# Kernel tuning notes

Hardware: AMD Instinct MI355X
Metric: run time of the kernel (lower is better)

The kernel has to match this reference:

```python
import jax, jax.numpy as jnp
import numpy as np

THRESH = 0.4


def setup_inputs() -> dict:
    key = jax.random.key(0)
    ks = jax.random.split(key, 8)
    B, N, C, H, O = 8, 16384, 640, 256, 128
    s = 0.02  # small init so sigmoid(logits) ~ 0.5 -> realistic mixed selection
    return {
        "point_features": jax.random.normal(ks[0], (B, N, C), jnp.float32),
        "point_coords": jax.random.normal(ks[1], (B, N, 3), jnp.float32) * 10.0,
        "w1": jax.random.normal(ks[2], (C, H), jnp.float32) * s,
        "b1": jnp.zeros((H,), jnp.float32),
        "w2": jax.random.normal(ks[3], (H, 1), jnp.float32) * s,
        "b2": jnp.zeros((1,), jnp.float32),
        "wo": jax.random.normal(ks[4], (C, O), jnp.float32) * s,
        "bo": jnp.zeros((O,), jnp.float32),
    }


def reference(point_features, point_coords, w1, b1, w2, b2, wo, bo):
    B, N, _ = point_features.shape
    # 2-layer MLP -> per-point logit -> sigmoid score
    h = jax.nn.relu(jnp.einsum('bnc,ch->bnh', point_features, w1) + b1)
    logits = jnp.einsum('bnh,ho->bno', h, w2) + b2          # [B, N, 1]
    scores = jax.nn.sigmoid(logits)                          # [B, N, 1]
    # score-scaled features through output projection
    feats = jnp.einsum('bnc,co->bno', point_features * scores, wo) + bo  # [B, N, O]
    # score-threshold selection + per-batch stream compaction into a
    # zero-padded tensor (padded to N, the jit-static worst case)
    sel = scores[..., 0] > THRESH                            # [B, N] bool
    pos = jnp.cumsum(sel.astype(jnp.int32), axis=1) - 1      # destination slot
    pos = jnp.where(sel, pos, N)                             # unselected -> OOB (dropped)
    bidx = jnp.arange(B)[:, None]
    selected_keypoints = jnp.zeros_like(feats).at[bidx, pos].set(feats, mode='drop')
    selected_coords = jnp.zeros_like(point_coords).at[bidx, pos].set(point_coords, mode='drop')
    # point_mask: True where the row is zero padding (matches (coords==0).sum(-1)!=0)
    point_mask = jnp.sum(selected_coords == 0, axis=-1) != 0
    return selected_keypoints, selected_coords, point_mask
```

## Files before the change

### kernel.cpp

```cpp
#include <hip/hip_runtime.h>
#include <hip/hip_bf16.h>


typedef __attribute__((ext_vector_type(8))) short short8v;
typedef __attribute__((ext_vector_type(4))) float f32x4;

#define M_TOTAL 131072
#define C_DIM 640
#define H_DIM 256
#define O_DIM 128
#define NCOMB 384
#define TM 64
#define KSTEPS 20
#define N_PTS 16384
#define TILES_PER_B 256
#define NTILES 2048
#define THRL -0.4054651081f
#define FIX_MARGIN 0.03f

#define OUT_COORD_OFF 16777216
#define OUT_MASK_OFF  17170432

#define WT_OFF     0u
#define TMASK_OFF  491520u
#define TAGG_OFF   507904u
#define TEXCL_OFF  516096u
#define COUNTS_OFF 524288u
#define G_OFF      1572864u

#define LGKMCNT0 asm volatile("s_waitcnt lgkmcnt(0)" ::: "memory")
#define SBAR __builtin_amdgcn_s_barrier()

__device__ __forceinline__ unsigned int f2bf_bits(float f) {
  unsigned int u = __builtin_bit_cast(unsigned int, f);
  return (u + 0x7fffu + ((u >> 16) & 1u)) >> 16;
}
__device__ __forceinline__ unsigned int pack_bf2(float lo, float hi) {
  return f2bf_bits(lo) | (f2bf_bits(hi) << 16);
}

__global__ __launch_bounds__(256) void convert_w(const float* __restrict__ w1,
                                                 const float* __restrict__ wo,
                                                 unsigned short* __restrict__ Wt2) {
  int o = blockIdx.x * 256 + threadIdx.x;
  if (o < NCOMB * C_DIM) {
    int e = o & 7;
    int g = o >> 3;
    int pp = g & 3;
    int qq = (g >> 2) & 15;
    int tc = g >> 6;
    int ct = tc % 24;
    int t = tc / 24;
    int k = t * 32 + pp * 8 + e;
    int n = ct * 16 + qq;
    float v = (n < H_DIM) ? w1[k * H_DIM + n] : wo[k * O_DIM + (n - H_DIM)];
    Wt2[o] = (unsigned short)f2bf_bits(v);
  }
}

__global__ __launch_bounds__(512, 4) void gemm_fused(
    const float* __restrict__ pf, const unsigned short* __restrict__ Wt2,
    const float* __restrict__ w1, const float* __restrict__ b1,
    const float* __restrict__ w2, const float* __restrict__ b2,
    const float* __restrict__ bo, unsigned long long* __restrict__ tmask,
    int* __restrict__ tagg, float* __restrict__ G) {
  __shared__ __align__(16) unsigned short As[3][2048];

  const int tid = threadIdx.x;
  const int lane = tid & 63;
  const int wv = tid >> 6;
  const int q = lane & 15;
  const int p = lane >> 4;
  const int tile = blockIdx.x;
  const int m0 = tile * TM;

  f32x4 acc[3][4];
#pragma unroll
  for (int i = 0; i < 3; ++i)
#pragma unroll
    for (int rt = 0; rt < 4; ++rt) acc[i][rt] = (f32x4){0.f, 0.f, 0.f, 0.f};

  const float* asrc = pf + (size_t)(m0 + (tid >> 3)) * C_DIM + (tid & 7) * 4;
  const int aphys = ((tid >> 1) ^ ((tid >> 4) & 3)) * 8 + (tid & 1) * 4;
  const int aswz = (q >> 1) & 3;

  const unsigned short* bbase = Wt2 + wv * 512 + q * 32 + p * 8;

  float4 Rcur;
  {
    float4 R0 = *(const float4*)(asrc);
    Rcur = *(const float4*)(asrc + 32);
    *(uint2*)&As[0][aphys] = make_uint2(pack_bf2(R0.x, R0.y), pack_bf2(R0.z, R0.w));
    LGKMCNT0;
    SBAR;
  }

  int scur = 0;
#pragma unroll 1
  for (int t = 0; t < KSTEPS; ++t) {
    const unsigned short* bp = bbase + (size_t)t * 12288;
    short8v bc0 = *(const short8v*)(bp);
    short8v bc1 = *(const short8v*)(bp + 4096);
    short8v bc2 = *(const short8v*)(bp + 8192);
    int snxt = scur + 1;
    if (snxt == 3) snxt = 0;
    if (t + 2 < KSTEPS) {
      float4 Rnext = *(const float4*)(asrc + (t + 2) * 32);
      *(uint2*)&As[snxt][aphys] =
          make_uint2(pack_bf2(Rcur.x, Rcur.y), pack_bf2(Rcur.z, Rcur.w));
      Rcur = Rnext;
    } else if (t + 1 < KSTEPS) {
      *(uint2*)&As[snxt][aphys] =
          make_uint2(pack_bf2(Rcur.x, Rcur.y), pack_bf2(Rcur.z, Rcur.w));
    }
    LGKMCNT0;
    SBAR;
    short8v af[4];
#pragma unroll
    for (int rt = 0; rt < 4; ++rt)
      af[rt] = *(const short8v*)&As[scur][((rt * 64 + q * 4 + p) ^ aswz) * 8];
    __builtin_amdgcn_s_setprio(1);
#pragma unroll
    for (int rt = 0; rt < 4; ++rt) {
      acc[0][rt] = __builtin_amdgcn_mfma_f32_16x16x32_bf16(af[rt], bc0, acc[0][rt], 0, 0, 0);
      acc[1][rt] = __builtin_amdgcn_mfma_f32_16x16x32_bf16(af[rt], bc1, acc[1][rt], 0, 0, 0);
      acc[2][rt] = __builtin_amdgcn_mfma_f32_16x16x32_bf16(af[rt], bc2, acc[2][rt], 0, 0, 0);
    }
    __builtin_amdgcn_s_setprio(0);
    scur = snxt;
  }
  __syncthreads();

  float* lpart = (float*)&As[0][0];
  float* llog = (float*)&As[1][0];
  float* srow = llog + 64;
  float* fsum = srow + 64;
  unsigned long long* s_fixmask = (unsigned long long*)(fsum + 4);

  float w2v[2], b1v[2];
#pragma unroll
  for (int i = 0; i < 2; ++i) {
    int col = (wv + 8 * i) * 16 + q;
    w2v[i] = w2[col];
    b1v[i] = b1[col];
  }
#pragma unroll
  for (int rt = 0; rt < 4; ++rt) {
    float pr[4] = {0.f, 0.f, 0.f, 0.f};
#pragma unroll
    for (int i = 0; i < 2; ++i)
#pragma unroll
      for (int r = 0; r < 4; ++r)
        pr[r] += fmaxf(acc[i][rt][r] + b1v[i], 0.f) * w2v[i];
#pragma unroll
    for (int mk = 1; mk < 16; mk <<= 1)
#pragma unroll
      for (int r = 0; r < 4; ++r) pr[r] += __shfl_xor(pr[r], mk);
    if (q == 0)
#pragma unroll
      for (int r = 0; r < 4; ++r) lpart[wv * 64 + rt * 16 + p * 4 + r] = pr[r];
  }
  __syncthreads();

  bool nf = false;
  if (wv == 0) {
    float lg = b2[0];
#pragma unroll
    for (int w = 0; w < 8; ++w) lg += lpart[w * 64 + tid];
    llog[tid] = lg;
    nf = fabsf(lg - THRL) < FIX_MARGIN;
  }
  unsigned long long fm = __ballot(nf);
  if (tid == 0) *s_fixmask = fm;
  __syncthreads();

  unsigned long long fixmask = *s_fixmask;
  while (fixmask) {
    int row = __ffsll(fixmask) - 1;
    fixmask &= fixmask - 1;
    if (tid < 256) {
      const float* prow = pf + (size_t)(m0 + row) * C_DIM;
      float a0 = 0.f, a1 = 0.f;
      for (int c = 0; c < C_DIM; c += 2) {
        a0 = fmaf(prow[c], w1[(size_t)c * H_DIM + tid], a0);
        a1 = fmaf(prow[c + 1], w1[(size_t)(c + 1) * H_DIM + tid], a1);
      }
      float v = fmaxf(a0 + a1 + b1[tid], 0.f) * w2[tid];
#pragma unroll
      for (int mk = 1; mk < 64; mk <<= 1) v += __shfl_xor(v, mk);
      if (lane == 0) fsum[wv] = v;
    }
    __syncthreads();
    if (tid == 0)
      llog[row] = fsum[0] + fsum[1] + fsum[2] + fsum[3] + b2[0];
    __syncthreads();
  }

  bool sel = false;
  float flog = 0.f;
  if (wv == 0) {
    flog = llog[tid];
    sel = flog > THRL;
  }
  unsigned long long selmask = __ballot(sel);
  if (wv == 0) {
    srow[tid] = 1.f / (1.f + expf(-flog));
    if (tid == 0) {
      tmask[tile] = selmask;
      tagg[tile] = __popcll(selmask);
    }
  }
  __syncthreads();

  {
    const int gcol = wv * 16 + q;
    const float bov = bo[gcol];
#pragma unroll
    for (int rt = 0; rt < 4; ++rt)
#pragma unroll
      for (int r = 0; r < 4; ++r) {
        int row = rt * 16 + p * 4 + r;
        G[(size_t)(m0 + row) * O_DIM + gcol] = fmaf(acc[2][rt][r], srow[row], bov);
      }
  }
}

__global__ __launch_bounds__(256) void scan_tiles(const int* __restrict__ tagg,
                                                  int* __restrict__ texcl,
                                                  int* __restrict__ counts) {
  __shared__ int wsum[4];
  const int c = blockIdx.x, t = threadIdx.x;
  const int lane = t & 63, w = t >> 6;
  int v = tagg[c * 256 + t];
  int inc = v;
#pragma unroll
  for (int d = 1; d < 64; d <<= 1) {
    int n = __shfl_up(inc, d);
    if (lane >= d) inc += n;
  }
  if (lane == 63) wsum[w] = inc;
  __syncthreads();
  int base = 0;
#pragma unroll
  for (int ww = 0; ww < 4; ++ww)
    if (ww < w) base += wsum[ww];
  texcl[c * 256 + t] = base + inc - v;
  if (t == 255) counts[c] = base + inc;
}

__global__ __launch_bounds__(512) void scatter(
    const float* __restrict__ G, const unsigned long long* __restrict__ tmask,
    const int* __restrict__ texcl, const float* __restrict__ pc,
    float* __restrict__ out) {
  const int tile = blockIdx.x;
  const int tid = threadIdx.x;
  const int lane = tid & 63;
  const int wv = tid >> 6;
  const unsigned long long mask = tmask[tile];
  const int base = (tile >> 8) * N_PTS + texcl[tile];
  const int m0 = tile * TM;
#pragma unroll
  for (int j = 0; j < 8; ++j) {
    const int row = wv * 8 + j;
    if (!((mask >> row) & 1ull)) continue;
    const int dst = base + __popcll(mask & ((1ull << row) - 1ull));
    const int m = m0 + row;
    float2 g = *(const float2*)(G + (size_t)m * O_DIM + lane * 2);
    *(float2*)(out + (size_t)dst * O_DIM + lane * 2) = g;
    if (lane == 0) {
      float c0 = pc[m * 3], c1 = pc[m * 3 + 1], c2 = pc[m * 3 + 2];
      float* oc = out + OUT_COORD_OFF;
      oc[dst * 3] = c0; oc[dst * 3 + 1] = c1; oc[dst * 3 + 2] = c2;
      out[OUT_MASK_OFF + dst] = (c0 == 0.f || c1 == 0.f || c2 == 0.f) ? 1.f : 0.f;
    }
  }
}

__global__ __launch_bounds__(256) void fill_tail(const int* __restrict__ counts,
                                                 float* __restrict__ out) {
  const int lane = threadIdx.x & 63;
  for (int m = blockIdx.x * 4 + (threadIdx.x >> 6); m < M_TOTAL; m += 8192) {
    int b = m >> 14, j = m & (N_PTS - 1);
    if (j < counts[b]) continue;
    *(float2*)(out + (size_t)m * O_DIM + lane * 2) = make_float2(0.f, 0.f);
    if (lane == 0) {
      float* oc = out + OUT_COORD_OFF;
      oc[m * 3] = 0.f; oc[m * 3 + 1] = 0.f; oc[m * 3 + 2] = 0.f;
      out[OUT_MASK_OFF + m] = 1.f;
    }
  }
}

extern "C" void kernel_launch(void* const* d_in, const int* in_sizes, int n_in,
                              void* d_out, int out_size, void* d_ws, size_t ws_size,
                              hipStream_t stream) {
  const float* pf = (const float*)d_in[0];
  const float* pc = (const float*)d_in[1];
  const float* w1 = (const float*)d_in[2];
  const float* b1 = (const float*)d_in[3];
  const float* w2 = (const float*)d_in[4];
  const float* b2 = (const float*)d_in[5];
  const float* wo = (const float*)d_in[6];
  const float* bo = (const float*)d_in[7];
  float* out = (float*)d_out;
  char* ws = (char*)d_ws;

  unsigned short* Wt2 = (unsigned short*)(ws + WT_OFF);
  unsigned long long* tmask = (unsigned long long*)(ws + TMASK_OFF);
  int* tagg = (int*)(ws + TAGG_OFF);
  int* texcl = (int*)(ws + TEXCL_OFF);
  int* counts = (int*)(ws + COUNTS_OFF);
  float* G = (float*)(ws + G_OFF);

  convert_w<<<960, 256, 0, stream>>>(w1, wo, Wt2);
  gemm_fused<<<NTILES, 512, 0, stream>>>(pf, Wt2, w1, b1, w2, b2, bo,
                                         tmask, tagg, G);
  scan_tiles<<<8, 256, 0, stream>>>(tagg, texcl, counts);
  scatter<<<NTILES, 512, 0, stream>>>(G, tmask, texcl, pc, out);
  fill_tail<<<2048, 256, 0, stream>>>(counts, out);
}
```

Baseline: 197.5 us.

## Switch fused GEMM to FP8 MFMA with register-resident weights and persistent blocks

Weights are quantized to FP8 (scaled by 64) and activations are converted to FP8 on the fly, so the GEMM uses 16x16x32 fp8 MFMA instead of bf16. Each of 256 persistent blocks of 768 threads keeps its full K slice of weights in registers and loops over eight 64-row tiles. The aim is to cut weight reloads and halve LDS and MFMA operand width. The cost is lower precision, which is offset by widening the exact-recompute margin near the threshold, plus much higher register pressure.

```diff
diff --git a/kernel.cpp b/kernel.cpp
--- a/kernel.cpp
+++ b/kernel.cpp
@@ -2,227 +2,230 @@
 #include <hip/hip_bf16.h>
 
 
-typedef __attribute__((ext_vector_type(8))) short short8v;
 typedef __attribute__((ext_vector_type(4))) float f32x4;
 
 #define M_TOTAL 131072
 #define C_DIM 640
 #define H_DIM 256
 #define O_DIM 128
-#define NCOMB 384
-#define TM 64
-#define KSTEPS 20
+#define KS 20
 #define N_PTS 16384
-#define TILES_PER_B 256
-#define NTILES 2048
+#define NBLOCKS 256
+#define NCHUNKS 2048
 #define THRL -0.4054651081f
-#define FIX_MARGIN 0.03f
+#define FIX_MARGIN 0.08f
+#define INV64 0.015625f
 
 #define OUT_COORD_OFF 16777216
 #define OUT_MASK_OFF  17170432
 
 #define WT_OFF     0u
-#define TMASK_OFF  491520u
-#define TAGG_OFF   507904u
-#define TEXCL_OFF  516096u
-#define COUNTS_OFF 524288u
+#define TMASK_OFF  262144u
+#define TAGG_OFF   278528u
+#define TEXCL_OFF  286720u
+#define COUNTS_OFF 294912u
 #define G_OFF      1572864u
 
 #define LGKMCNT0 asm volatile("s_waitcnt lgkmcnt(0)" ::: "memory")
 #define SBAR __builtin_amdgcn_s_barrier()
 
-__device__ __forceinline__ unsigned int f2bf_bits(float f) {
-  unsigned int u = __builtin_bit_cast(unsigned int, f);
-  return (u + 0x7fffu + ((u >> 16) & 1u)) >> 16;
-}
-__device__ __forceinline__ unsigned int pack_bf2(float lo, float hi) {
-  return f2bf_bits(lo) | (f2bf_bits(hi) << 16);
-}
-
 __global__ __launch_bounds__(256) void convert_w(const float* __restrict__ w1,
                                                  const float* __restrict__ wo,
-                                                 unsigned short* __restrict__ Wt2) {
-  int o = blockIdx.x * 256 + threadIdx.x;
-  if (o < NCOMB * C_DIM) {
-    int e = o & 7;
-    int g = o >> 3;
-    int pp = g & 3;
-    int qq = (g >> 2) & 15;
-    int tc = g >> 6;
-    int ct = tc % 24;
-    int t = tc / 24;
-    int k = t * 32 + pp * 8 + e;
-    int n = ct * 16 + qq;
-    float v = (n < H_DIM) ? w1[k * H_DIM + n] : wo[k * O_DIM + (n - H_DIM)];
-    Wt2[o] = (unsigned short)f2bf_bits(v);
-  }
-}
-
-__global__ __launch_bounds__(512, 4) void gemm_fused(
-    const float* __restrict__ pf, const unsigned short* __restrict__ Wt2,
+                                                 unsigned int* __restrict__ Wu) {
+  int i = blockIdx.x * 256 + threadIdx.x;
+  if (i >= 61440) return;
+  int g = i >> 1, h = i & 1;
+  int p = g & 3, q = (g >> 2) & 15, tc = g >> 6;
+  int ct = tc % 24, t = tc / 24;
+  int n = ct * 16 + q;
+  int kb = t * 32 + p * 8 + h * 4;
+  float v[4];
+#pragma unroll
+  for (int e = 0; e < 4; ++e) {
+    int k = kb + e;
+    v[e] = ((n < H_DIM) ? w1[k * H_DIM + n] : wo[k * O_DIM + (n - H_DIM)]) * 64.f;
+  }
+  unsigned int u = __builtin_amdgcn_cvt_pk_fp8_f32(v[0], v[1], 0, false);
+  u = __builtin_amdgcn_cvt_pk_fp8_f32(v[2], v[3], u, true);
+  Wu[i] = u;
+}
+
+__global__ __launch_bounds__(768, 3) void gemm_fused(
+    const float* __restrict__ pf, const unsigned char* __restrict__ Wf8,
     const float* __restrict__ w1, const float* __restrict__ b1,
     const float* __restrict__ w2, const float* __restrict__ b2,
     const float* __restrict__ bo, unsigned long long* __restrict__ tmask,
     int* __restrict__ tagg, float* __restrict__ G) {
-  __shared__ __align__(16) unsigned short As[3][2048];
+  __shared__ __align__(16) unsigned char As[3][2048];
+  __shared__ float lpart[8][64];
+  __shared__ float llog[64];
+  __shared__ float srow[64];
+  __shared__ float fsum[4];
+  __shared__ unsigned long long s_fm;
 
   const int tid = threadIdx.x;
   const int lane = tid & 63;
   const int wv = tid >> 6;
   const int q = lane & 15;
   const int p = lane >> 4;
-  const int tile = blockIdx.x;
-  const int m0 = tile * TM;
-
-  f32x4 acc[3][4];
-#pragma unroll
-  for (int i = 0; i < 3; ++i)
-#pragma unroll
-    for (int rt = 0; rt < 4; ++rt) acc[i][rt] = (f32x4){0.f, 0.f, 0.f, 0.f};
-
-  const float* asrc = pf + (size_t)(m0 + (tid >> 3)) * C_DIM + (tid & 7) * 4;
-  const int aphys = ((tid >> 1) ^ ((tid >> 4) & 3)) * 8 + (tid & 1) * 4;
-  const int aswz = (q >> 1) & 3;
-
-  const unsigned short* bbase = Wt2 + wv * 512 + q * 32 + p * 8;
-
-  float4 Rcur;
-  {
-    float4 R0 = *(const float4*)(asrc);
-    Rcur = *(const float4*)(asrc + 32);
-    *(uint2*)&As[0][aphys] = make_uint2(pack_bf2(R0.x, R0.y), pack_bf2(R0.z, R0.w));
+  const int blk = blockIdx.x;
+
+  const char* bb = (const char*)Wf8 + (size_t)(q * 4 + p) * 8 + (size_t)(2 * wv) * 512;
+  long B0[KS], B1[KS];
+#pragma unroll
+  for (int t = 0; t < KS; ++t) {
+    B0[t] = *(const long*)(bb + (size_t)t * 12288);
+    B1[t] = *(const long*)(bb + (size_t)t * 12288 + 512);
+  }
+
+  const int row_s = tid >> 3;
+  const int kh = tid & 7;
+  const int wboff = ((((kh >> 1) << 6) + row_s) ^ (kh >> 1)) * 8 + (kh & 1) * 4;
+
+#define STW(SLOT, F)                                                          \
+  {                                                                           \
+    unsigned int u_ = __builtin_amdgcn_cvt_pk_fp8_f32((F).x, (F).y, 0, false);\
+    u_ = __builtin_amdgcn_cvt_pk_fp8_f32((F).z, (F).w, u_, true);             \
+    *(unsigned int*)&As[SLOT][wboff] = u_;                                    \
+  }
+
+#pragma unroll 1
+  for (int mt = 0; mt < 8; ++mt) {
+    const int m0 = blk * 512 + mt * 64;
+    const float* asrc = pf + (size_t)(m0 + row_s) * C_DIM + kh * 4;
+
+    f32x4 acc[2][4];
+#pragma unroll
+    for (int i = 0; i < 2; ++i)
+#pragma unroll
+      for (int rt = 0; rt < 4; ++rt) acc[i][rt] = (f32x4){0.f, 0.f, 0.f, 0.f};
+
+    float4 pipe[4];
+    if (tid < 512) {
+      pipe[0] = *(const float4*)(asrc);
+      pipe[1] = *(const float4*)(asrc + 32);
+      pipe[2] = *(const float4*)(asrc + 64);
+      STW(0, pipe[0]);
+    }
     LGKMCNT0;
     SBAR;
-  }
-
-  int scur = 0;
-#pragma unroll 1
-  for (int t = 0; t < KSTEPS; ++t) {
-    const unsigned short* bp = bbase + (size_t)t * 12288;
-    short8v bc0 = *(const short8v*)(bp);
-    short8v bc1 = *(const short8v*)(bp + 4096);
-    short8v bc2 = *(const short8v*)(bp + 8192);
-    int snxt = scur + 1;
-    if (snxt == 3) snxt = 0;
-    if (t + 2 < KSTEPS) {
-      float4 Rnext = *(const float4*)(asrc + (t + 2) * 32);
-      *(uint2*)&As[snxt][aphys] =
-          make_uint2(pack_bf2(Rcur.x, Rcur.y), pack_bf2(Rcur.z, Rcur.w));
-      Rcur = Rnext;
-    } else if (t + 1 < KSTEPS) {
-      *(uint2*)&As[snxt][aphys] =
-          make_uint2(pack_bf2(Rcur.x, Rcur.y), pack_bf2(Rcur.z, Rcur.w));
-    }
-    LGKMCNT0;
-    SBAR;
-    short8v af[4];
-#pragma unroll
-    for (int rt = 0; rt < 4; ++rt)
-      af[rt] = *(const short8v*)&As[scur][((rt * 64 + q * 4 + p) ^ aswz) * 8];
-    __builtin_amdgcn_s_setprio(1);
-#pragma unroll
-    for (int rt = 0; rt < 4; ++rt) {
-      acc[0][rt] = __builtin_amdgcn_mfma_f32_16x16x32_bf16(af[rt], bc0, acc[0][rt], 0, 0, 0);
-      acc[1][rt] = __builtin_amdgcn_mfma_f32_16x16x32_bf16(af[rt], bc1, acc[1][rt], 0, 0, 0);
-      acc[2][rt] = __builtin_amdgcn_mfma_f32_16x16x32_bf16(af[rt], bc2, acc[2][rt], 0, 0, 0);
-    }
-    __builtin_amdgcn_s_setprio(0);
-    scur = snxt;
-  }
-  __syncthreads();
-
-  float* lpart = (float*)&As[0][0];
-  float* llog = (float*)&As[1][0];
-  float* srow = llog + 64;
-  float* fsum = srow + 64;
-  unsigned long long* s_fixmask = (unsigned long long*)(fsum + 4);
-
-  float w2v[2], b1v[2];
-#pragma unroll
-  for (int i = 0; i < 2; ++i) {
-    int col = (wv + 8 * i) * 16 + q;
-    w2v[i] = w2[col];
-    b1v[i] = b1[col];
-  }
-#pragma unroll
-  for (int rt = 0; rt < 4; ++rt) {
-    float pr[4] = {0.f, 0.f, 0.f, 0.f};
-#pragma unroll
-    for (int i = 0; i < 2; ++i)
-#pragma unroll
-      for (int r = 0; r < 4; ++r)
-        pr[r] += fmaxf(acc[i][rt][r] + b1v[i], 0.f) * w2v[i];
-#pragma unroll
-    for (int mk = 1; mk < 16; mk <<= 1)
-#pragma unroll
-      for (int r = 0; r < 4; ++r) pr[r] += __shfl_xor(pr[r], mk);
-    if (q == 0)
-#pragma unroll
-      for (int r = 0; r < 4; ++r) lpart[wv * 64 + rt * 16 + p * 4 + r] = pr[r];
-  }
-  __syncthreads();
-
-  bool nf = false;
-  if (wv == 0) {
-    float lg = b2[0];
-#pragma unroll
-    for (int w = 0; w < 8; ++w) lg += lpart[w * 64 + tid];
-    llog[tid] = lg;
-    nf = fabsf(lg - THRL) < FIX_MARGIN;
-  }
-  unsigned long long fm = __ballot(nf);
-  if (tid == 0) *s_fixmask = fm;
-  __syncthreads();
-
-  unsigned long long fixmask = *s_fixmask;
-  while (fixmask) {
-    int row = __ffsll(fixmask) - 1;
-    fixmask &= fixmask - 1;
-    if (tid < 256) {
-      const float* prow = pf + (size_t)(m0 + row) * C_DIM;
-      float a0 = 0.f, a1 = 0.f;
-      for (int c = 0; c < C_DIM; c += 2) {
-        a0 = fmaf(prow[c], w1[(size_t)c * H_DIM + tid], a0);
-        a1 = fmaf(prow[c + 1], w1[(size_t)(c + 1) * H_DIM + tid], a1);
-      }
-      float v = fmaxf(a0 + a1 + b1[tid], 0.f) * w2[tid];
-#pragma unroll
-      for (int mk = 1; mk < 64; mk <<= 1) v += __shfl_xor(v, mk);
-      if (lane == 0) fsum[wv] = v;
-    }
-    __syncthreads();
-    if (tid == 0)
-      llog[row] = fsum[0] + fsum[1] + fsum[2] + fsum[3] + b2[0];
-    __syncthreads();
-  }
-
-  bool sel = false;
-  float flog = 0.f;
-  if (wv == 0) {
-    flog = llog[tid];
-    sel = flog > THRL;
-  }
-  unsigned long long selmask = __ballot(sel);
-  if (wv == 0) {
-    srow[tid] = 1.f / (1.f + expf(-flog));
+
+#pragma unroll
+    for (int t = 0; t < KS; ++t) {
+      if (tid < 512) {
+        if (t + 3 < KS) pipe[(t + 3) & 3] = *(const float4*)(asrc + (t + 3) * 32);
+        if (t + 1 < KS) STW((t + 1) % 3, pipe[(t + 1) & 3]);
+      }
+      LGKMCNT0;
+      SBAR;
+      long a0 = *(const long*)&As[t % 3][((p * 64 + 0 * 16 + q) ^ p) * 8];
+      long a1 = *(const long*)&As[t % 3][((p * 64 + 1 * 16 + q) ^ p) * 8];
+      long a2 = *(const long*)&As[t % 3][((p * 64 + 2 * 16 + q) ^ p) * 8];
+      long a3 = *(const long*)&As[t % 3][((p * 64 + 3 * 16 + q) ^ p) * 8];
+      acc[0][0] = __builtin_amdgcn_mfma_f32_16x16x32_fp8_fp8(a0, B0[t], acc[0][0], 0, 0, 0);
+      acc[1][0] = __builtin_amdgcn_mfma_f32_16x16x32_fp8_fp8(a0, B1[t], acc[1][0], 0, 0, 0);
+      acc[0][1] = __builtin_amdgcn_mfma_f32_16x16x32_fp8_fp8(a1, B0[t], acc[0][1], 0, 0, 0);
+      acc[1][1] = __builtin_amdgcn_mfma_f32_16x16x32_fp8_fp8(a1, B1[t], acc[1][1], 0, 0, 0);
+      acc[0][2] = __builtin_amdgcn_mfma_f32_16x16x32_fp8_fp8(a2, B0[t], acc[0][2], 0, 0, 0);
+      acc[1][2] = __builtin_amdgcn_mfma_f32_16x16x32_fp8_fp8(a2, B1[t], acc[1][2], 0, 0, 0);
+      acc[0][3] = __builtin_amdgcn_mfma_f32_16x16x32_fp8_fp8(a3, B0[t], acc[0][3], 0, 0, 0);
+      acc[1][3] = __builtin_amdgcn_mfma_f32_16x16x32_fp8_fp8(a3, B1[t], acc[1][3], 0, 0, 0);
+    }
+    __syncthreads();
+
+    if (wv < 8) {
+      float b1v[2], w2v[2];
+#pragma unroll
+      for (int i = 0; i < 2; ++i) {
+        int col = (2 * wv + i) * 16 + q;
+        b1v[i] = b1[col];
+        w2v[i] = w2[col];
+      }
+#pragma unroll
+      for (int rt = 0; rt < 4; ++rt) {
+        float pr[4] = {0.f, 0.f, 0.f, 0.f};
+#pragma unroll
+        for (int i = 0; i < 2; ++i)
+#pragma unroll
+          for (int r = 0; r < 4; ++r)
+            pr[r] += fmaxf(acc[i][rt][r] * INV64 + b1v[i], 0.f) * w2v[i];
+#pragma unroll
+        for (int mk = 1; mk < 16; mk <<= 1)
+#pragma unroll
+          for (int r = 0; r < 4; ++r) pr[r] += __shfl_xor(pr[r], mk);
+        if (q == 0)
+#pragma unroll
+          for (int r = 0; r < 4; ++r) lpart[wv][rt * 16 + p * 4 + r] = pr[r];
+      }
+    }
+    __syncthreads();
+
+    bool nf = false;
+    if (tid < 64) {
+      float lg = b2[0];
+#pragma unroll
+      for (int w = 0; w < 8; ++w) lg += lpart[w][tid];
+      llog[tid] = lg;
+      nf = fabsf(lg - THRL) < FIX_MARGIN;
+    }
+    unsigned long long fm = __ballot(nf);
+    if (tid == 0) s_fm = fm;
+    __syncthreads();
+
+    unsigned long long fixmask = s_fm;
+    while (fixmask) {
+      int row = __ffsll(fixmask) - 1;
+      fixmask &= fixmask - 1;
+      if (tid < 256) {
+        const float* prow = pf + (size_t)(m0 + row) * C_DIM;
+        float a0 = 0.f, a1 = 0.f;
+        for (int c = 0; c < C_DIM; c += 2) {
+          a0 = fmaf(prow[c], w1[(size_t)c * H_DIM + tid], a0);
+          a1 = fmaf(prow[c + 1], w1[(size_t)(c + 1) * H_DIM + tid], a1);
+        }
+        float v = fmaxf(a0 + a1 + b1[tid], 0.f) * w2[tid];
+#pragma unroll
+        for (int mk = 1; mk < 64; mk <<= 1) v += __shfl_xor(v, mk);
+        if (lane == 0) fsum[tid >> 6] = v;
+      }
+      __syncthreads();
+      if (tid == 0)
+        llog[row] = fsum[0] + fsum[1] + fsum[2] + fsum[3] + b2[0];
+      __syncthreads();
+    }
+
+    bool sel = false;
+    if (tid < 64) {
+      float flog = llog[tid];
+      sel = flog > THRL;
+      srow[tid] = 1.f / (1.f + expf(-flog));
+    }
+    unsigned long long mk2 = __ballot(sel);
     if (tid == 0) {
-      tmask[tile] = selmask;
-      tagg[tile] = __popcll(selmask);
-    }
-  }
-  __syncthreads();
-
-  {
-    const int gcol = wv * 16 + q;
-    const float bov = bo[gcol];
-#pragma unroll
-    for (int rt = 0; rt < 4; ++rt)
-#pragma unroll
-      for (int r = 0; r < 4; ++r) {
-        int row = rt * 16 + p * 4 + r;
-        G[(size_t)(m0 + row) * O_DIM + gcol] = fmaf(acc[2][rt][r], srow[row], bov);
-      }
-  }
+      int ch = blk * 8 + mt;
+      tmask[ch] = mk2;
+      tagg[ch] = __popcll(mk2);
+    }
+    __syncthreads();
+
+    if (wv >= 8) {
+#pragma unroll
+      for (int i = 0; i < 2; ++i) {
+        int gcol = ((wv - 8) * 2 + i) * 16 + q;
+        float bov = bo[gcol];
+#pragma unroll
+        for (int rt = 0; rt < 4; ++rt)
+#pragma unroll
+          for (int r = 0; r < 4; ++r) {
+            int row = rt * 16 + p * 4 + r;
+            G[(size_t)(m0 + row) * O_DIM + gcol] =
+                fmaf(acc[i][rt][r] * INV64, srow[row], bov);
+          }
+      }
+    }
+    __syncthreads();
+  }
+#undef STW
 }
 
 __global__ __launch_bounds__(256) void scan_tiles(const int* __restrict__ tagg,
@@ -252,13 +255,13 @@
     const float* __restrict__ G, const unsigned long long* __restrict__ tmask,
     const int* __restrict__ texcl, const float* __restrict__ pc,
     float* __restrict__ out) {
-  const int tile = blockIdx.x;
+  const int ch = blockIdx.x;
   const int tid = threadIdx.x;
   const int lane = tid & 63;
   const int wv = tid >> 6;
-  const unsigned long long mask = tmask[tile];
-  const int base = (tile >> 8) * N_PTS + texcl[tile];
-  const int m0 = tile * TM;
+  const unsigned long long mask = tmask[ch];
+  const int base = (ch >> 8) * N_PTS + texcl[ch];
+  const int m0 = ch * 64;
 #pragma unroll
   for (int j = 0; j < 8; ++j) {
     const int row = wv * 8 + j;
@@ -305,17 +308,17 @@
   float* out = (float*)d_out;
   char* ws = (char*)d_ws;
 
-  unsigned short* Wt2 = (unsigned short*)(ws + WT_OFF);
+  unsigned int* Wu = (unsigned int*)(ws + WT_OFF);
   unsigned long long* tmask = (unsigned long long*)(ws + TMASK_OFF);
   int* tagg = (int*)(ws + TAGG_OFF);
   int* texcl = (int*)(ws + TEXCL_OFF);
   int* counts = (int*)(ws + COUNTS_OFF);
   float* G = (float*)(ws + G_OFF);
 
-  convert_w<<<960, 256, 0, stream>>>(w1, wo, Wt2);
-  gemm_fused<<<NTILES, 512, 0, stream>>>(pf, Wt2, w1, b1, w2, b2, bo,
-                                         tmask, tagg, G);
+  convert_w<<<240, 256, 0, stream>>>(w1, wo, Wu);
+  gemm_fused<<<NBLOCKS, 768, 0, stream>>>(pf, (const unsigned char*)Wu, w1, b1,
+                                          w2, b2, bo, tmask, tagg, G);
   scan_tiles<<<8, 256, 0, stream>>>(tagg, texcl, counts);
-  scatter<<<NTILES, 512, 0, stream>>>(G, tmask, texcl, pc, out);
+  scatter<<<NCHUNKS, 512, 0, stream>>>(G, tmask, texcl, pc, out);
   fill_tail<<<2048, 256, 0, stream>>>(counts, out);
 }
```

After: 529.1 us. +168.0%, slower.
